# Kernel optimization log

Hardware: AMD Instinct MI355X
Metric: run time of the kernel (lower is better)

The kernel has to match this reference:

```python
import jax, jax.numpy as jnp
import numpy as np

B, L, R, DV = 4, 4096, 8, 64

def setup_inputs() -> dict:
    key = jax.random.key(0)
    k1, k2, k3, k4 = jax.random.split(key, 4)
    return {
        "v": jax.random.normal(k1, (B, L, DV), dtype=jnp.float32),
        "mask": jax.random.randint(k2, (B, 1, L), 0, 2, dtype=jnp.int32),
        "random_attn_1": jax.random.normal(k3, (B, L, R), dtype=jnp.float32),
        "random_attn_2": jax.random.normal(k4, (B, R, L), dtype=jnp.float32),
        "len_q": L,
    }

def reference(v, mask, random_attn_1, random_attn_2, len_q):
    # rank-8 low-rank synthesis of attention scores: [B, len_q, len_q]
    Bm = mask.shape[0]
    scores = jnp.einsum("blr,brm->blm",
                        random_attn_1[:Bm, :len_q, :],
                        random_attn_2[:Bm, :, :len_q])
    scores = jnp.where(mask == 0, jnp.float32(-1e9), scores)
    attn = jax.nn.softmax(scores, axis=-1)  # dropout omitted (eval mode)
    out = jnp.einsum("blm,bmd->bld", attn, v[:Bm, :len_q, :])
    return out, attn
```

## Files before the change

### kernel.cpp

```cpp
#include <hip/hip_runtime.h>
#include <hip/hip_bf16.h>

#define BB  4
#define LL  4096
#define RR  8
#define DVV 64

typedef __bf16 bf16x8 __attribute__((ext_vector_type(8)));
typedef float  f32x4  __attribute__((ext_vector_type(4)));

__global__ __launch_bounds__(256) void prep_kernel(
    const float* __restrict__ v, __bf16* __restrict__ vF) {
  __shared__ __bf16 tl[64][72];
  const int blk = blockIdx.x;
  const int b   = blk >> 6;
  const int m0  = (blk & 63) << 6;
  const int tid = threadIdx.x;

  const float* vb = v + (((size_t)(b * LL + m0)) << 6);
#pragma unroll
  for (int i = 0; i < 16; ++i) {
    const int idx = (i << 8) + tid;
    tl[idx & 63][idx >> 6] = (__bf16)vb[idx];
  }
  __syncthreads();

  const int wv = tid >> 6, ln = tid & 63;
#pragma unroll
  for (int i = 0; i < 2; ++i) {
    const int u  = wv + (i << 2);
    const int cb = u >> 2, gg = u & 3;
    const int d  = gg * 16 + (ln & 15);
    const int c  = cb * 32 + ((ln >> 4) << 3);
    const size_t unit = ((size_t)(b * 128 + (m0 >> 5) + cb) << 2) + gg;
    *(bf16x8*)(vF + (unit << 9) + (ln << 3)) = *(const bf16x8*)&tl[d][c];
  }
}

__global__ __launch_bounds__(512, 4) void attn_main(
    const float* __restrict__ ra1, const float* __restrict__ ra2,
    const int* __restrict__ mask, const __bf16* __restrict__ vF,
    float* __restrict__ out, float* __restrict__ attn) {
  __shared__ __bf16 pbuf[8 * 8 * 512];
  __shared__ float  red[8 * 8];

  const int wg   = blockIdx.x;
  const int b    = wg >> 9;
  const int row0 = (wg & 511) << 3;
  const int tid  = threadIdx.x;
  const int wave = tid >> 6;
  const int lane = tid & 63;
  const int col0 = (wave << 9) + (lane << 3);

  const float* r2 = ra2 + (size_t)b * (RR * LL) + col0;
  f32x4 rlo[RR], rhi[RR];
#pragma unroll
  for (int r = 0; r < RR; ++r) {
    rlo[r] = *(const f32x4*)(r2 + r * LL);
    rhi[r] = *(const f32x4*)(r2 + r * LL + 4);
  }
  const int* mp = mask + (size_t)b * LL + col0;
  f32x4 mlo, mhi;
#pragma unroll
  for (int j = 0; j < 4; ++j) {
    mlo[j] = mp[j]     ? 1.0f : 0.0f;
    mhi[j] = mp[4 + j] ? 1.0f : 0.0f;
  }

  const float* a_base = ra1 + ((size_t)b * LL + row0) * RR;
  char* const  pw     = (char*)pbuf + (wave << 13);

  float part[8];
#pragma unroll
  for (int i = 0; i < 8; ++i) {
    const float* ap = a_base + i * RR;
    f32x4 slo = {0.f, 0.f, 0.f, 0.f}, shi = {0.f, 0.f, 0.f, 0.f};
#pragma unroll
    for (int r = 0; r < RR; ++r) {
      const float a = ap[r];
#pragma unroll
      for (int j = 0; j < 4; ++j) {
        slo[j] = fmaf(a, rlo[r][j], slo[j]);
        shi[j] = fmaf(a, rhi[r][j], shi[j]);
      }
    }
    float e[8];
#pragma unroll
    for (int j = 0; j < 4; ++j) {
      e[j]     = __expf(slo[j]) * mlo[j];
      e[4 + j] = __expf(shi[j]) * mhi[j];
    }
    part[i] = ((e[0] + e[1]) + (e[2] + e[3])) + ((e[4] + e[5]) + (e[6] + e[7]));

    bf16x8 pe;
#pragma unroll
    for (int j = 0; j < 8; ++j) pe[j] = (__bf16)e[j];
    *(bf16x8*)(pw + (i << 10) + ((lane << 4) ^ ((i & 7) << 4))) = pe;
  }
#pragma unroll
  for (int s = 1; s < 64; s <<= 1)
#pragma unroll
    for (int i = 0; i < 8; ++i) part[i] += __shfl_xor(part[i], s);
  if (lane == 0) {
#pragma unroll
    for (int i = 0; i < 8; ++i) red[wave * 8 + i] = part[i];
  }
  __syncthreads();

  float* attn_base = attn + ((size_t)b * LL + row0) * LL + col0;
#pragma unroll 2
  for (int i = 0; i < 8; ++i) {
    float rt = 0.f;
#pragma unroll
    for (int w = 0; w < 8; ++w) rt += red[w * 8 + i];
    const float rinv = 1.0f / rt;
    const bf16x8 pe =
        *(const bf16x8*)(pw + (i << 10) + ((lane << 4) ^ ((i & 7) << 4)));
    f32x4 o0, o1;
#pragma unroll
    for (int j = 0; j < 4; ++j) {
      o0[j] = (float)pe[j] * rinv;
      o1[j] = (float)pe[4 + j] * rinv;
    }
    __builtin_nontemporal_store(o0, (f32x4*)(attn_base + (size_t)i * LL));
    __builtin_nontemporal_store(o1, (f32x4*)(attn_base + (size_t)i * LL + 4));
  }

  const int lrow = lane & 15, kg = lane >> 4;
  const int lr8  = lrow & 7;
  f32x4 acc[4];
#pragma unroll
  for (int g = 0; g < 4; ++g) acc[g] = (f32x4){0.f, 0.f, 0.f, 0.f};
  const __bf16* vFb = vF + ((size_t)b << 18);
#pragma unroll 4
  for (int t = 0; t < 16; ++t) {
    const bf16x8 af = *(const bf16x8*)(
        pw + (lr8 << 10) + (((t << 6) + (kg << 4)) ^ (lr8 << 4)));
    const __bf16* vblk = vFb + ((size_t)((wave << 4) + t) << 11) + (lane << 3);
#pragma unroll
    for (int g = 0; g < 4; ++g) {
      const bf16x8 bf = *(const bf16x8*)(vblk + (g << 9));
      acc[g] = __builtin_amdgcn_mfma_f32_16x16x32_bf16(af, bf, acc[g], 0, 0, 0);
    }
  }

  asm volatile("s_waitcnt lgkmcnt(0)\n\ts_barrier" ::: "memory");
  float* osum = (float*)pbuf;
  if (kg < 2) {
#pragma unroll
    for (int g = 0; g < 4; ++g)
#pragma unroll
      for (int ii = 0; ii < 4; ++ii)
        osum[(wave * 8 + kg * 4 + ii) * 64 + g * 16 + lrow] = acc[g][ii];
  }
  asm volatile("s_waitcnt lgkmcnt(0)\n\ts_barrier" ::: "memory");

  if (tid < 128) {
    const int orow = tid >> 4;
    const int d    = (tid & 15) << 2;
    f32x4 o = {0.f, 0.f, 0.f, 0.f};
#pragma unroll
    for (int w = 0; w < 8; ++w) {
      const f32x4 rr = *(const f32x4*)(osum + ((w * 8 + orow) << 6) + d);
#pragma unroll
      for (int j = 0; j < 4; ++j) o[j] += rr[j];
    }
    float rt = 0.f;
#pragma unroll
    for (int w = 0; w < 8; ++w) rt += red[w * 8 + orow];
    const float rinv = 1.0f / rt;
#pragma unroll
    for (int j = 0; j < 4; ++j) o[j] *= rinv;
    *(f32x4*)(out + ((size_t)b * LL + row0 + orow) * DVV + d) = o;
  }
}

extern "C" void kernel_launch(void* const* d_in, const int* in_sizes, int n_in,
                              void* d_out, int out_size, void* d_ws,
                              size_t ws_size, hipStream_t stream) {
  (void)in_sizes; (void)n_in; (void)out_size; (void)ws_size;
  const float* v    = (const float*)d_in[0];
  const int*   mask = (const int*)d_in[1];
  const float* ra1  = (const float*)d_in[2];
  const float* ra2  = (const float*)d_in[3];

  float* out  = (float*)d_out;
  float* attn = out + (size_t)BB * LL * DVV;

  __bf16* vF = (__bf16*)d_ws;

  hipLaunchKernelGGL(prep_kernel, dim3(BB * (LL / 64)), dim3(256), 0, stream,
                     v, vF);
  hipLaunchKernelGGL(attn_main, dim3(BB * LL / 8), dim3(512), 0, stream,
                     ra1, ra2, mask, vF, out, attn);
}
```

Measured before the change: 356.8 us.

## Interleave attn stores with PV MFMA loop and coalesce column mapping

Each lane now owns two 4-wide column groups 256 apart instead of one contiguous 8-wide group, which makes the ra2, mask and attn accesses of a wave contiguous 1 KB segments. The attn normalization and store loop is folded into the P·V MFMA loop, so the global stores of each row are issued between the matrix ops. This is meant to overlap the heavy attn write traffic with compute. Row-sum reductions are transposed so they can be read with vector loads. The cost is more LDS accesses, since the probabilities are now written and read as bf16x4 halves, and higher register pressure from unrolling.

```diff
diff --git a/kernel.cpp b/kernel.cpp
--- a/kernel.cpp
+++ b/kernel.cpp
@@ -7,7 +7,9 @@
 #define DVV 64
 
 typedef __bf16 bf16x8 __attribute__((ext_vector_type(8)));
+typedef __bf16 bf16x4 __attribute__((ext_vector_type(4)));
 typedef float  f32x4  __attribute__((ext_vector_type(4)));
+typedef int    i32x4  __attribute__((ext_vector_type(4)));
 
 __global__ __launch_bounds__(256) void prep_kernel(
     const float* __restrict__ v, __bf16* __restrict__ vF) {
@@ -42,7 +44,7 @@
     const int* __restrict__ mask, const __bf16* __restrict__ vF,
     float* __restrict__ out, float* __restrict__ attn) {
   __shared__ __bf16 pbuf[8 * 8 * 512];
-  __shared__ float  red[8 * 8];
+  __shared__ float  red[8][8];
 
   const int wg   = blockIdx.x;
   const int b    = wg >> 9;
@@ -50,21 +52,23 @@
   const int tid  = threadIdx.x;
   const int wave = tid >> 6;
   const int lane = tid & 63;
-  const int col0 = (wave << 9) + (lane << 3);
-
-  const float* r2 = ra2 + (size_t)b * (RR * LL) + col0;
-  f32x4 rlo[RR], rhi[RR];
+  const int W    = wave << 9;
+
+  const float* r2 = ra2 + (size_t)b * (RR * LL) + W + (lane << 2);
+  f32x4 rA[RR], rB[RR];
 #pragma unroll
   for (int r = 0; r < RR; ++r) {
-    rlo[r] = *(const f32x4*)(r2 + r * LL);
-    rhi[r] = *(const f32x4*)(r2 + r * LL + 4);
-  }
-  const int* mp = mask + (size_t)b * LL + col0;
-  f32x4 mlo, mhi;
+    rA[r] = *(const f32x4*)(r2 + r * LL);
+    rB[r] = *(const f32x4*)(r2 + r * LL + 256);
+  }
+  const int* mp = mask + (size_t)b * LL + W + (lane << 2);
+  const i32x4 mAv = *(const i32x4*)mp;
+  const i32x4 mBv = *(const i32x4*)(mp + 256);
+  f32x4 mA, mB;
 #pragma unroll
   for (int j = 0; j < 4; ++j) {
-    mlo[j] = mp[j]     ? 1.0f : 0.0f;
-    mhi[j] = mp[4 + j] ? 1.0f : 0.0f;
+    mA[j] = mAv[j] ? 1.0f : 0.0f;
+    mB[j] = mBv[j] ? 1.0f : 0.0f;
   }
 
   const float* a_base = ra1 + ((size_t)b * LL + row0) * RR;
@@ -74,28 +78,31 @@
 #pragma unroll
   for (int i = 0; i < 8; ++i) {
     const float* ap = a_base + i * RR;
-    f32x4 slo = {0.f, 0.f, 0.f, 0.f}, shi = {0.f, 0.f, 0.f, 0.f};
+    f32x4 sA = {0.f, 0.f, 0.f, 0.f}, sB = {0.f, 0.f, 0.f, 0.f};
 #pragma unroll
     for (int r = 0; r < RR; ++r) {
       const float a = ap[r];
 #pragma unroll
       for (int j = 0; j < 4; ++j) {
-        slo[j] = fmaf(a, rlo[r][j], slo[j]);
-        shi[j] = fmaf(a, rhi[r][j], shi[j]);
+        sA[j] = fmaf(a, rA[r][j], sA[j]);
+        sB[j] = fmaf(a, rB[r][j], sB[j]);
       }
     }
-    float e[8];
+    f32x4 eA, eB;
 #pragma unroll
     for (int j = 0; j < 4; ++j) {
-      e[j]     = __expf(slo[j]) * mlo[j];
-      e[4 + j] = __expf(shi[j]) * mhi[j];
-    }
-    part[i] = ((e[0] + e[1]) + (e[2] + e[3])) + ((e[4] + e[5]) + (e[6] + e[7]));
-
-    bf16x8 pe;
-#pragma unroll
-    for (int j = 0; j < 8; ++j) pe[j] = (__bf16)e[j];
-    *(bf16x8*)(pw + (i << 10) + ((lane << 4) ^ ((i & 7) << 4))) = pe;
+      eA[j] = __expf(sA[j]) * mA[j];
+      eB[j] = __expf(sB[j]) * mB[j];
+    }
+    part[i] = ((eA[0] + eA[1]) + (eA[2] + eA[3])) +
+              ((eB[0] + eB[1]) + (eB[2] + eB[3]));
+
+    bf16x4 pA, pB;
+#pragma unroll
+    for (int j = 0; j < 4; ++j) { pA[j] = (__bf16)eA[j]; pB[j] = (__bf16)eB[j]; }
+    const int swz = (i & 7) << 4;
+    *(bf16x4*)(pw + (i << 10) + (((lane << 3)) ^ swz))       = pA;
+    *(bf16x4*)(pw + (i << 10) + ((512 + (lane << 3)) ^ swz)) = pB;
   }
 #pragma unroll
   for (int s = 1; s < 64; s <<= 1)
@@ -103,27 +110,17 @@
     for (int i = 0; i < 8; ++i) part[i] += __shfl_xor(part[i], s);
   if (lane == 0) {
 #pragma unroll
-    for (int i = 0; i < 8; ++i) red[wave * 8 + i] = part[i];
+    for (int i = 0; i < 8; ++i) red[i][wave] = part[i];
   }
   __syncthreads();
 
-  float* attn_base = attn + ((size_t)b * LL + row0) * LL + col0;
-#pragma unroll 2
+  float rinv[8];
+#pragma unroll
   for (int i = 0; i < 8; ++i) {
-    float rt = 0.f;
-#pragma unroll
-    for (int w = 0; w < 8; ++w) rt += red[w * 8 + i];
-    const float rinv = 1.0f / rt;
-    const bf16x8 pe =
-        *(const bf16x8*)(pw + (i << 10) + ((lane << 4) ^ ((i & 7) << 4)));
-    f32x4 o0, o1;
-#pragma unroll
-    for (int j = 0; j < 4; ++j) {
-      o0[j] = (float)pe[j] * rinv;
-      o1[j] = (float)pe[4 + j] * rinv;
-    }
-    __builtin_nontemporal_store(o0, (f32x4*)(attn_base + (size_t)i * LL));
-    __builtin_nontemporal_store(o1, (f32x4*)(attn_base + (size_t)i * LL + 4));
+    const f32x4 r0 = *(const f32x4*)&red[i][0];
+    const f32x4 r1 = *(const f32x4*)&red[i][4];
+    rinv[i] = 1.0f / (((r0[0] + r0[1]) + (r0[2] + r0[3])) +
+                      ((r1[0] + r1[1]) + (r1[2] + r1[3])));
   }
 
   const int lrow = lane & 15, kg = lane >> 4;
@@ -132,16 +129,37 @@
 #pragma unroll
   for (int g = 0; g < 4; ++g) acc[g] = (f32x4){0.f, 0.f, 0.f, 0.f};
   const __bf16* vFb = vF + ((size_t)b << 18);
-#pragma unroll 4
-  for (int t = 0; t < 16; ++t) {
-    const bf16x8 af = *(const bf16x8*)(
-        pw + (lr8 << 10) + (((t << 6) + (kg << 4)) ^ (lr8 << 4)));
-    const __bf16* vblk = vFb + ((size_t)((wave << 4) + t) << 11) + (lane << 3);
-#pragma unroll
-    for (int g = 0; g < 4; ++g) {
-      const bf16x8 bf = *(const bf16x8*)(vblk + (g << 9));
-      acc[g] = __builtin_amdgcn_mfma_f32_16x16x32_bf16(af, bf, acc[g], 0, 0, 0);
-    }
+  float* attn_base  = attn + ((size_t)b * LL + row0) * LL + W + (lane << 2);
+
+#pragma unroll
+  for (int i = 0; i < 8; ++i) {
+#pragma unroll
+    for (int h = 0; h < 2; ++h) {
+      const int t = 2 * i + h;
+      const bf16x8 af = *(const bf16x8*)(
+          pw + (lr8 << 10) + (((t << 6) + (kg << 4)) ^ (lr8 << 4)));
+      const __bf16* vblk =
+          vFb + ((size_t)((wave << 4) + t) << 11) + (lane << 3);
+#pragma unroll
+      for (int g = 0; g < 4; ++g) {
+        const bf16x8 bf = *(const bf16x8*)(vblk + (g << 9));
+        acc[g] =
+            __builtin_amdgcn_mfma_f32_16x16x32_bf16(af, bf, acc[g], 0, 0, 0);
+      }
+    }
+    const int swz = (i & 7) << 4;
+    const bf16x4 pA =
+        *(const bf16x4*)(pw + (i << 10) + (((lane << 3)) ^ swz));
+    const bf16x4 pB =
+        *(const bf16x4*)(pw + (i << 10) + ((512 + (lane << 3)) ^ swz));
+    f32x4 oA, oB;
+#pragma unroll
+    for (int j = 0; j < 4; ++j) {
+      oA[j] = (float)pA[j] * rinv[i];
+      oB[j] = (float)pB[j] * rinv[i];
+    }
+    __builtin_nontemporal_store(oA, (f32x4*)(attn_base + (size_t)i * LL));
+    __builtin_nontemporal_store(oB, (f32x4*)(attn_base + (size_t)i * LL + 256));
   }
 
   asm volatile("s_waitcnt lgkmcnt(0)\n\ts_barrier" ::: "memory");
@@ -167,10 +185,10 @@
     }
     float rt = 0.f;
 #pragma unroll
-    for (int w = 0; w < 8; ++w) rt += red[w * 8 + orow];
-    const float rinv = 1.0f / rt;
-#pragma unroll
-    for (int j = 0; j < 4; ++j) o[j] *= rinv;
+    for (int w = 0; w < 8; ++w) rt += red[orow][w];
+    const float rinv_o = 1.0f / rt;
+#pragma unroll
+    for (int j = 0; j < 4; ++j) o[j] *= rinv_o;
     *(f32x4*)(out + ((size_t)b * LL + row0 + orow) * DVV + d) = o;
   }
 }
```

New measurement: 316.5 us. 1.13x faster.
